# Kernel optimization log

Hardware: AMD Instinct MI355X
Metric: run time of the kernel (lower is better)

The kernel has to match this reference:

```python
import jax, jax.numpy as jnp
import numpy as np

B, TE, TD, H = 8, 512, 256, 256  # batch, enc len, dec len, hidden (He==Hd)

def setup_inputs() -> dict:
    key = jax.random.key(0)
    k1, k2, k3, k4, k5 = jax.random.split(key, 5)
    # Keras 'uniform' initializer: U(-0.05, 0.05)
    u = lambda k, s: jax.random.uniform(k, s, jnp.float32, -0.05, 0.05)
    return {
        "encoder_out_seq": jax.random.normal(k1, (B, TE, H), jnp.float32),
        "decoder_out_seq": jax.random.normal(k2, (B, TD, H), jnp.float32),
        "W_a": u(k3, (H, H)),
        "U_a": u(k4, (H, H)),
        "V_a": u(k5, (H, 1)),
    }

def reference(encoder_out_seq, decoder_out_seq, W_a, U_a, V_a):
    # Bahdanau additive attention, fully batched (same math as the per-step K.rnn loop)
    We = jnp.einsum('bih,hk->bik', encoder_out_seq, W_a)   # [B,Te,H]
    Uh = jnp.einsum('bjh,hk->bjk', decoder_out_seq, U_a)   # [B,Td,H]
    # energies: V_a^T tanh(We_i + Uh_j)  -> [B,Td,Te]
    t = jnp.tanh(We[:, None, :, :] + Uh[:, :, None, :])    # [B,Td,Te,H]
    e = jnp.einsum('bjih,h->bji', t, V_a[:, 0])             # [B,Td,Te]
    e = jax.nn.softmax(e, axis=-1)                          # softmax over encoder positions
    c = jnp.einsum('bji,bih->bjh', e, encoder_out_seq)      # [B,Td,H]
    return (c, e)
```

## Files before the change

### kernel.cpp

```cpp
#include <hip/hip_runtime.h>


#define BB 8
#define TE 512
#define TD 256
#define HH 256

#define EXP2F(x) __builtin_amdgcn_exp2f(x)
#define RCPF(x)  __builtin_amdgcn_rcpf(x)
#define KSCALE   2.8853900817779268f
#define NSC      (-2.8853900817779268f)

__global__ __launch_bounds__(256) void k_pre(
    const float* __restrict__ enc, const float* __restrict__ dec,
    const float* __restrict__ Wa,  const float* __restrict__ Ua,
    float* __restrict__ WeT, float* __restrict__ Uh)
{
    const int tid = threadIdx.x;
    const bool is_enc = blockIdx.x < 256;
    const int bi = is_enc ? blockIdx.x : (blockIdx.x - 256);
    const int m0 = (bi >> 2) * 64;
    const int n0 = (bi & 3) * 64;
    const float* X = is_enc ? enc : dec;
    const float* W = is_enc ? Wa : Ua;

    __shared__ float Xs[32][68];
    __shared__ float Ws[32][68];

    const int kq = tid & 7,  xr = tid >> 3;
    const int wk = tid >> 3, wn = (tid & 7) * 8;
    const int tx = tid & 15, ty = tid >> 4;

    float acc[4][4];
    #pragma unroll
    for (int r = 0; r < 4; r++)
        #pragma unroll
        for (int c = 0; c < 4; c++) acc[r][c] = 0.f;

    for (int kc = 0; kc < HH; kc += 32) {
        float4 xa = *(const float4*)(X + (size_t)(m0 + xr) * HH + kc + kq * 4);
        float4 xb = *(const float4*)(X + (size_t)(m0 + xr + 32) * HH + kc + kq * 4);
        float4 wa = *(const float4*)(W + (size_t)(kc + wk) * HH + n0 + wn);
        float4 wb = *(const float4*)(W + (size_t)(kc + wk) * HH + n0 + wn + 4);
        __syncthreads();
        Xs[kq * 4 + 0][xr] = xa.x; Xs[kq * 4 + 1][xr] = xa.y;
        Xs[kq * 4 + 2][xr] = xa.z; Xs[kq * 4 + 3][xr] = xa.w;
        Xs[kq * 4 + 0][xr + 32] = xb.x; Xs[kq * 4 + 1][xr + 32] = xb.y;
        Xs[kq * 4 + 2][xr + 32] = xb.z; Xs[kq * 4 + 3][xr + 32] = xb.w;
        *(float4*)&Ws[wk][wn]     = wa;
        *(float4*)&Ws[wk][wn + 4] = wb;
        __syncthreads();
        #pragma unroll
        for (int k = 0; k < 32; k++) {
            float4 a = *(const float4*)&Xs[k][ty * 4];
            float4 b = *(const float4*)&Ws[k][tx * 4];
            acc[0][0] = fmaf(a.x, b.x, acc[0][0]); acc[0][1] = fmaf(a.x, b.y, acc[0][1]);
            acc[0][2] = fmaf(a.x, b.z, acc[0][2]); acc[0][3] = fmaf(a.x, b.w, acc[0][3]);
            acc[1][0] = fmaf(a.y, b.x, acc[1][0]); acc[1][1] = fmaf(a.y, b.y, acc[1][1]);
            acc[1][2] = fmaf(a.y, b.z, acc[1][2]); acc[1][3] = fmaf(a.y, b.w, acc[1][3]);
            acc[2][0] = fmaf(a.z, b.x, acc[2][0]); acc[2][1] = fmaf(a.z, b.y, acc[2][1]);
            acc[2][2] = fmaf(a.z, b.z, acc[2][2]); acc[2][3] = fmaf(a.z, b.w, acc[2][3]);
            acc[3][0] = fmaf(a.w, b.x, acc[3][0]); acc[3][1] = fmaf(a.w, b.y, acc[3][1]);
            acc[3][2] = fmaf(a.w, b.z, acc[3][2]); acc[3][3] = fmaf(a.w, b.w, acc[3][3]);
        }
    }

    if (is_enc) {
        const int b  = m0 >> 9;
        const int ib = (m0 & 511) + ty * 4;
        #pragma unroll
        for (int c = 0; c < 4; c++) {
            float4 v;
            v.x = EXP2F(acc[0][c] * KSCALE); v.y = EXP2F(acc[1][c] * KSCALE);
            v.z = EXP2F(acc[2][c] * KSCALE); v.w = EXP2F(acc[3][c] * KSCALE);
            *(float4*)(WeT + ((size_t)b * HH + n0 + tx * 4 + c) * TE + ib) = v;
        }
    } else {
        #pragma unroll
        for (int r = 0; r < 4; r++) {
            float4 v;
            v.x = EXP2F(acc[r][0] * KSCALE); v.y = EXP2F(acc[r][1] * KSCALE);
            v.z = EXP2F(acc[r][2] * KSCALE); v.w = EXP2F(acc[r][3] * KSCALE);
            *(float4*)(Uh + (size_t)(m0 + ty * 4 + r) * HH + n0 + tx * 4) = v;
        }
    }
}

__global__ __launch_bounds__(512) void k_attn(
    const float* __restrict__ enc, const float* __restrict__ WeT,
    const float* __restrict__ Uhe, const float* __restrict__ Va,
    float* __restrict__ out_c, float* __restrict__ out_e)
{
    const int wv = threadIdx.x >> 6, lane = threadIdx.x & 63;
    const int b   = blockIdx.x >> 6;
    const int j0  = (blockIdx.x & 63) * 4;
    const int jj0 = b * TD + j0;

    __shared__ float sP[TE][4];
    __shared__ float sR[8][4][HH];

    const int i = (wv << 6) + lane;
    const float* wt = WeT + (size_t)b * HH * TE + i;
    const float* ut = Uhe + (size_t)jj0 * HH;

    float a0 = 0.f, a1 = 0.f, a2 = 0.f, a3 = 0.f;
    #pragma unroll 4
    for (int h = 0; h < HH; h++) {
        float vah = Va[h];
        float u_0 = ut[h];
        float u_1 = ut[HH + h];
        float u_2 = ut[2 * HH + h];
        float u_3 = ut[3 * HH + h];
        float w = wt[(size_t)h * TE];
        a0 = fmaf(vah, RCPF(fmaf(w, u_0, 1.f)), a0);
        a1 = fmaf(vah, RCPF(fmaf(w, u_1, 1.f)), a1);
        a2 = fmaf(vah, RCPF(fmaf(w, u_2, 1.f)), a2);
        a3 = fmaf(vah, RCPF(fmaf(w, u_3, 1.f)), a3);
    }
    float4 E; E.x = NSC * a0; E.y = NSC * a1; E.z = NSC * a2; E.w = NSC * a3;
    *(float4*)&sP[i][0] = E;
    __syncthreads();

    if (wv < 4) {
        float ev[8];
        float m = -3.0e38f;
        #pragma unroll
        for (int k = 0; k < 8; k++) {
            ev[k] = sP[lane + 64 * k][wv];
            m = fmaxf(m, ev[k]);
        }
        #pragma unroll
        for (int off = 32; off; off >>= 1) m = fmaxf(m, __shfl_xor(m, off, 64));
        float s = 0.f;
        #pragma unroll
        for (int k = 0; k < 8; k++) { ev[k] = EXP2F(ev[k] - m); s += ev[k]; }
        #pragma unroll
        for (int off = 32; off; off >>= 1) s += __shfl_xor(s, off, 64);
        float rs = RCPF(s);
        float* oe = out_e + (size_t)(jj0 + wv) * TE;
        #pragma unroll
        for (int k = 0; k < 8; k++) {
            float p = ev[k] * rs;
            sP[lane + 64 * k][wv] = p;
            oe[lane + 64 * k] = p;
        }
    }
    __syncthreads();

    const float* eb = enc + ((size_t)b * TE + (wv << 6)) * HH + 4 * lane;
    float4 c0 = {0,0,0,0}, c1 = {0,0,0,0}, c2 = {0,0,0,0}, c3 = {0,0,0,0};
    #pragma unroll 2
    for (int k = 0; k < 64; k++) {
        float4 p = *(const float4*)&sP[(wv << 6) + k][0];
        float4 q = *(const float4*)(eb + (size_t)k * HH);
        c0.x = fmaf(p.x, q.x, c0.x); c0.y = fmaf(p.x, q.y, c0.y);
        c0.z = fmaf(p.x, q.z, c0.z); c0.w = fmaf(p.x, q.w, c0.w);
        c1.x = fmaf(p.y, q.x, c1.x); c1.y = fmaf(p.y, q.y, c1.y);
        c1.z = fmaf(p.y, q.z, c1.z); c1.w = fmaf(p.y, q.w, c1.w);
        c2.x = fmaf(p.z, q.x, c2.x); c2.y = fmaf(p.z, q.y, c2.y);
        c2.z = fmaf(p.z, q.z, c2.z); c2.w = fmaf(p.z, q.w, c2.w);
        c3.x = fmaf(p.w, q.x, c3.x); c3.y = fmaf(p.w, q.y, c3.y);
        c3.z = fmaf(p.w, q.z, c3.z); c3.w = fmaf(p.w, q.w, c3.w);
    }
    *(float4*)&sR[wv][0][4 * lane] = c0;
    *(float4*)&sR[wv][1][4 * lane] = c1;
    *(float4*)&sR[wv][2][4 * lane] = c2;
    *(float4*)&sR[wv][3][4 * lane] = c3;
    __syncthreads();

    {
        const int jr = wv & 3;
        const int h2 = (wv >> 2) * 128 + 2 * lane;
        float sx = 0.f, sy = 0.f;
        #pragma unroll
        for (int ww = 0; ww < 8; ww++) {
            float2 t = *(const float2*)&sR[ww][jr][h2];
            sx += t.x; sy += t.y;
        }
        float2 o; o.x = sx; o.y = sy;
        *(float2*)(out_c + (size_t)(jj0 + jr) * HH + h2) = o;
    }
}

extern "C" void kernel_launch(void* const* d_in, const int* in_sizes, int n_in,
                              void* d_out, int out_size, void* d_ws, size_t ws_size,
                              hipStream_t stream) {
    const float* enc = (const float*)d_in[0];
    const float* dec = (const float*)d_in[1];
    const float* Wa  = (const float*)d_in[2];
    const float* Ua  = (const float*)d_in[3];
    const float* Va  = (const float*)d_in[4];

    float* WeT = (float*)d_ws;
    float* Uhe = WeT + (size_t)BB * HH * TE;

    float* out_c = (float*)d_out;
    float* out_e = out_c + (size_t)BB * TD * HH;

    k_pre<<<384, 256, 0, stream>>>(enc, dec, Wa, Ua, WeT, Uhe);
    k_attn<<<BB * TD / 4, 512, 0, stream>>>(enc, WeT, Uhe, Va, out_c, out_e);
}
```

Measured before the change: 126.5 us.

## Interleave WeT in float4 h-groups and split H reduction across doubled waves

```diff
diff --git a/kernel.cpp b/kernel.cpp
--- a/kernel.cpp
+++ b/kernel.cpp
@@ -14,7 +14,7 @@
 __global__ __launch_bounds__(256) void k_pre(
     const float* __restrict__ enc, const float* __restrict__ dec,
     const float* __restrict__ Wa,  const float* __restrict__ Ua,
-    float* __restrict__ WeT, float* __restrict__ Uh)
+    float* __restrict__ W4, float* __restrict__ Uhe)
 {
     const int tid = threadIdx.x;
     const bool is_enc = blockIdx.x < 256;
@@ -68,26 +68,28 @@
     if (is_enc) {
         const int b  = m0 >> 9;
         const int ib = (m0 & 511) + ty * 4;
-        #pragma unroll
-        for (int c = 0; c < 4; c++) {
-            float4 v;
-            v.x = EXP2F(acc[0][c] * KSCALE); v.y = EXP2F(acc[1][c] * KSCALE);
-            v.z = EXP2F(acc[2][c] * KSCALE); v.w = EXP2F(acc[3][c] * KSCALE);
-            *(float4*)(WeT + ((size_t)b * HH + n0 + tx * 4 + c) * TE + ib) = v;
-        }
-    } else {
+        const int hq = (n0 >> 2) + tx;
+        float* dst = W4 + (((size_t)b * 64 + hq) * TE + ib) * 4;
         #pragma unroll
         for (int r = 0; r < 4; r++) {
             float4 v;
             v.x = EXP2F(acc[r][0] * KSCALE); v.y = EXP2F(acc[r][1] * KSCALE);
             v.z = EXP2F(acc[r][2] * KSCALE); v.w = EXP2F(acc[r][3] * KSCALE);
-            *(float4*)(Uh + (size_t)(m0 + ty * 4 + r) * HH + n0 + tx * 4) = v;
+            *(float4*)(dst + (size_t)r * 4) = v;
+        }
+    } else {
+        #pragma unroll
+        for (int r = 0; r < 4; r++) {
+            float4 v;
+            v.x = EXP2F(acc[r][0] * KSCALE); v.y = EXP2F(acc[r][1] * KSCALE);
+            v.z = EXP2F(acc[r][2] * KSCALE); v.w = EXP2F(acc[r][3] * KSCALE);
+            *(float4*)(Uhe + (size_t)(m0 + ty * 4 + r) * HH + n0 + tx * 4) = v;
         }
     }
 }
 
-__global__ __launch_bounds__(512) void k_attn(
-    const float* __restrict__ enc, const float* __restrict__ WeT,
+__global__ __launch_bounds__(1024, 8) void k_attn(
+    const float* __restrict__ enc, const float* __restrict__ W4,
     const float* __restrict__ Uhe, const float* __restrict__ Va,
     float* __restrict__ out_c, float* __restrict__ out_e)
 {
@@ -96,29 +98,45 @@
     const int j0  = (blockIdx.x & 63) * 4;
     const int jj0 = b * TD + j0;
 
-    __shared__ float sP[TE][4];
+    __shared__ float sE[2][TE][4];
     __shared__ float sR[8][4][HH];
 
-    const int i = (wv << 6) + lane;
-    const float* wt = WeT + (size_t)b * HH * TE + i;
-    const float* ut = Uhe + (size_t)jj0 * HH;
+    const int g   = wv >> 3;
+    const int i   = ((wv & 7) << 6) + lane;
+    const int hq0 = g * 32;
+
+    const float* wp = W4 + (((size_t)b * 64 + hq0) * TE + i) * 4;
+    const float* ua = Uhe + (size_t)jj0 * HH + hq0 * 4;
+    const float* va = Va + hq0 * 4;
 
     float a0 = 0.f, a1 = 0.f, a2 = 0.f, a3 = 0.f;
     #pragma unroll 4
-    for (int h = 0; h < HH; h++) {
-        float vah = Va[h];
-        float u_0 = ut[h];
-        float u_1 = ut[HH + h];
-        float u_2 = ut[2 * HH + h];
-        float u_3 = ut[3 * HH + h];
-        float w = wt[(size_t)h * TE];
-        a0 = fmaf(vah, RCPF(fmaf(w, u_0, 1.f)), a0);
-        a1 = fmaf(vah, RCPF(fmaf(w, u_1, 1.f)), a1);
-        a2 = fmaf(vah, RCPF(fmaf(w, u_2, 1.f)), a2);
-        a3 = fmaf(vah, RCPF(fmaf(w, u_3, 1.f)), a3);
+    for (int q = 0; q < 32; q++) {
+        float4 w4 = *(const float4*)(wp + (size_t)q * TE * 4);
+        float4 v4 = *(const float4*)(va + 4 * q);
+        float4 u0 = *(const float4*)(ua + 4 * q);
+        float4 u1 = *(const float4*)(ua + HH + 4 * q);
+        float4 u2 = *(const float4*)(ua + 2 * HH + 4 * q);
+        float4 u3 = *(const float4*)(ua + 3 * HH + 4 * q);
+        a0 = fmaf(v4.x, RCPF(fmaf(w4.x, u0.x, 1.f)), a0);
+        a0 = fmaf(v4.y, RCPF(fmaf(w4.y, u0.y, 1.f)), a0);
+        a0 = fmaf(v4.z, RCPF(fmaf(w4.z, u0.z, 1.f)), a0);
+        a0 = fmaf(v4.w, RCPF(fmaf(w4.w, u0.w, 1.f)), a0);
+        a1 = fmaf(v4.x, RCPF(fmaf(w4.x, u1.x, 1.f)), a1);
+        a1 = fmaf(v4.y, RCPF(fmaf(w4.y, u1.y, 1.f)), a1);
+        a1 = fmaf(v4.z, RCPF(fmaf(w4.z, u1.z, 1.f)), a1);
+        a1 = fmaf(v4.w, RCPF(fmaf(w4.w, u1.w, 1.f)), a1);
+        a2 = fmaf(v4.x, RCPF(fmaf(w4.x, u2.x, 1.f)), a2);
+        a2 = fmaf(v4.y, RCPF(fmaf(w4.y, u2.y, 1.f)), a2);
+        a2 = fmaf(v4.z, RCPF(fmaf(w4.z, u2.z, 1.f)), a2);
+        a2 = fmaf(v4.w, RCPF(fmaf(w4.w, u2.w, 1.f)), a2);
+        a3 = fmaf(v4.x, RCPF(fmaf(w4.x, u3.x, 1.f)), a3);
+        a3 = fmaf(v4.y, RCPF(fmaf(w4.y, u3.y, 1.f)), a3);
+        a3 = fmaf(v4.z, RCPF(fmaf(w4.z, u3.z, 1.f)), a3);
+        a3 = fmaf(v4.w, RCPF(fmaf(w4.w, u3.w, 1.f)), a3);
     }
     float4 E; E.x = NSC * a0; E.y = NSC * a1; E.z = NSC * a2; E.w = NSC * a3;
-    *(float4*)&sP[i][0] = E;
+    *(float4*)&sE[g][i][0] = E;
     __syncthreads();
 
     if (wv < 4) {
@@ -126,7 +144,8 @@
         float m = -3.0e38f;
         #pragma unroll
         for (int k = 0; k < 8; k++) {
-            ev[k] = sP[lane + 64 * k][wv];
+            int ii = lane + 64 * k;
+            ev[k] = sE[0][ii][wv] + sE[1][ii][wv];
             m = fmaxf(m, ev[k]);
         }
         #pragma unroll
@@ -141,17 +160,18 @@
         #pragma unroll
         for (int k = 0; k < 8; k++) {
             float p = ev[k] * rs;
-            sP[lane + 64 * k][wv] = p;
+            sE[0][lane + 64 * k][wv] = p;
             oe[lane + 64 * k] = p;
         }
     }
     __syncthreads();
 
-    const float* eb = enc + ((size_t)b * TE + (wv << 6)) * HH + 4 * lane;
+    const int ib = wv << 5;
+    const float* eb = enc + ((size_t)b * TE + ib) * HH + 4 * lane;
     float4 c0 = {0,0,0,0}, c1 = {0,0,0,0}, c2 = {0,0,0,0}, c3 = {0,0,0,0};
     #pragma unroll 2
-    for (int k = 0; k < 64; k++) {
-        float4 p = *(const float4*)&sP[(wv << 6) + k][0];
+    for (int k = 0; k < 32; k++) {
+        float4 p = *(const float4*)&sE[0][ib + k][0];
         float4 q = *(const float4*)(eb + (size_t)k * HH);
         c0.x = fmaf(p.x, q.x, c0.x); c0.y = fmaf(p.x, q.y, c0.y);
         c0.z = fmaf(p.x, q.z, c0.z); c0.w = fmaf(p.x, q.w, c0.w);
@@ -162,13 +182,31 @@
         c3.x = fmaf(p.w, q.x, c3.x); c3.y = fmaf(p.w, q.y, c3.y);
         c3.z = fmaf(p.w, q.z, c3.z); c3.w = fmaf(p.w, q.w, c3.w);
     }
-    *(float4*)&sR[wv][0][4 * lane] = c0;
-    *(float4*)&sR[wv][1][4 * lane] = c1;
-    *(float4*)&sR[wv][2][4 * lane] = c2;
-    *(float4*)&sR[wv][3][4 * lane] = c3;
-    __syncthreads();
-
-    {
+    if (wv < 8) {
+        *(float4*)&sR[wv][0][4 * lane] = c0;
+        *(float4*)&sR[wv][1][4 * lane] = c1;
+        *(float4*)&sR[wv][2][4 * lane] = c2;
+        *(float4*)&sR[wv][3][4 * lane] = c3;
+    }
+    __syncthreads();
+    if (wv >= 8) {
+        const int w8 = wv - 8;
+        float4 t;
+        t = *(const float4*)&sR[w8][0][4 * lane];
+        t.x += c0.x; t.y += c0.y; t.z += c0.z; t.w += c0.w;
+        *(float4*)&sR[w8][0][4 * lane] = t;
+        t = *(const float4*)&sR[w8][1][4 * lane];
+        t.x += c1.x; t.y += c1.y; t.z += c1.z; t.w += c1.w;
+        *(float4*)&sR[w8][1][4 * lane] = t;
+        t = *(const float4*)&sR[w8][2][4 * lane];
+        t.x += c2.x; t.y += c2.y; t.z += c2.z; t.w += c2.w;
+        *(float4*)&sR[w8][2][4 * lane] = t;
+        t = *(const float4*)&sR[w8][3][4 * lane];
+        t.x += c3.x; t.y += c3.y; t.z += c3.z; t.w += c3.w;
+        *(float4*)&sR[w8][3][4 * lane] = t;
+    }
+    __syncthreads();
+    if (wv < 8) {
         const int jr = wv & 3;
         const int h2 = (wv >> 2) * 128 + 2 * lane;
         float sx = 0.f, sy = 0.f;
@@ -191,12 +229,12 @@
     const float* Ua  = (const float*)d_in[3];
     const float* Va  = (const float*)d_in[4];
 
-    float* WeT = (float*)d_ws;
-    float* Uhe = WeT + (size_t)BB * HH * TE;
+    float* W4  = (float*)d_ws;
+    float* Uhe = W4 + (size_t)BB * HH * TE;
 
     float* out_c = (float*)d_out;
     float* out_e = out_c + (size_t)BB * TD * HH;
 
-    k_pre<<<384, 256, 0, stream>>>(enc, dec, Wa, Ua, WeT, Uhe);
-    k_attn<<<BB * TD / 4, 512, 0, stream>>>(enc, WeT, Uhe, Va, out_c, out_e);
+    k_pre<<<384, 256, 0, stream>>>(enc, dec, Wa, Ua, W4, Uhe);
+    k_attn<<<BB * TD / 4, 1024, 0, stream>>>(enc, W4, Uhe, Va, out_c, out_e);
 }
```

Result: slower. 189.8 us (+50.0%).

## Combine four reciprocal terms per division and use packed float2 FMAs

Applied to the files above, without the earlier changes.

```diff
diff --git a/kernel.cpp b/kernel.cpp
--- a/kernel.cpp
+++ b/kernel.cpp
@@ -11,10 +11,12 @@
 #define KSCALE   2.8853900817779268f
 #define NSC      (-2.8853900817779268f)
 
+typedef float v2f __attribute__((ext_vector_type(2)));
+
 __global__ __launch_bounds__(256) void k_pre(
     const float* __restrict__ enc, const float* __restrict__ dec,
     const float* __restrict__ Wa,  const float* __restrict__ Ua,
-    float* __restrict__ WeT, float* __restrict__ Uh)
+    float* __restrict__ W4, float* __restrict__ Uhe4)
 {
     const int tid = threadIdx.x;
     const bool is_enc = blockIdx.x < 256;
@@ -68,56 +70,83 @@
     if (is_enc) {
         const int b  = m0 >> 9;
         const int ib = (m0 & 511) + ty * 4;
+        const int hq = (n0 >> 2) + tx;
+        float* dst = W4 + (((size_t)b * 64 + hq) * TE + ib) * 4;
+        #pragma unroll
+        for (int r = 0; r < 4; r++) {
+            float4 v;
+            v.x = EXP2F(acc[r][0] * KSCALE); v.y = EXP2F(acc[r][1] * KSCALE);
+            v.z = EXP2F(acc[r][2] * KSCALE); v.w = EXP2F(acc[r][3] * KSCALE);
+            *(float4*)(dst + (size_t)r * 4) = v;
+        }
+    } else {
+        const int qd = (m0 + ty * 4) >> 2;
         #pragma unroll
         for (int c = 0; c < 4; c++) {
             float4 v;
             v.x = EXP2F(acc[0][c] * KSCALE); v.y = EXP2F(acc[1][c] * KSCALE);
             v.z = EXP2F(acc[2][c] * KSCALE); v.w = EXP2F(acc[3][c] * KSCALE);
-            *(float4*)(WeT + ((size_t)b * HH + n0 + tx * 4 + c) * TE + ib) = v;
-        }
-    } else {
-        #pragma unroll
-        for (int r = 0; r < 4; r++) {
-            float4 v;
-            v.x = EXP2F(acc[r][0] * KSCALE); v.y = EXP2F(acc[r][1] * KSCALE);
-            v.z = EXP2F(acc[r][2] * KSCALE); v.w = EXP2F(acc[r][3] * KSCALE);
-            *(float4*)(Uh + (size_t)(m0 + ty * 4 + r) * HH + n0 + tx * 4) = v;
-        }
-    }
+            *(float4*)(Uhe4 + ((size_t)qd * HH + n0 + tx * 4 + c) * 4) = v;
+        }
+    }
+}
+
+__device__ __forceinline__ v2f qstep2(const float4& w4, const float4& v4,
+                                      v2f u0, v2f u1, v2f u2, v2f u3, v2f acc)
+{
+    const v2f one = {1.f, 1.f};
+    v2f A = __builtin_elementwise_fma((v2f)(w4.x), u0, one);
+    v2f B = __builtin_elementwise_fma((v2f)(w4.y), u1, one);
+    v2f C = __builtin_elementwise_fma((v2f)(w4.z), u2, one);
+    v2f D = __builtin_elementwise_fma((v2f)(w4.w), u3, one);
+    v2f dAB = A * B, dCD = C * D;
+    v2f nAB = __builtin_elementwise_fma((v2f)(v4.x), B, (v2f)(v4.y) * A);
+    v2f nCD = __builtin_elementwise_fma((v2f)(v4.z), D, (v2f)(v4.w) * C);
+    v2f num = __builtin_elementwise_fma(nAB, dCD, nCD * dAB);
+    v2f den = dAB * dCD;
+    v2f r; r.x = RCPF(den.x); r.y = RCPF(den.y);
+    return __builtin_elementwise_fma(num, r, acc);
 }
 
 __global__ __launch_bounds__(512) void k_attn(
-    const float* __restrict__ enc, const float* __restrict__ WeT,
-    const float* __restrict__ Uhe, const float* __restrict__ Va,
+    const float* __restrict__ enc, const float* __restrict__ W4,
+    const float* __restrict__ Uhe4, const float* __restrict__ Va,
     float* __restrict__ out_c, float* __restrict__ out_e)
 {
     const int wv = threadIdx.x >> 6, lane = threadIdx.x & 63;
-    const int b   = blockIdx.x >> 6;
-    const int j0  = (blockIdx.x & 63) * 4;
+    const int b   = blockIdx.x & 7;
+    const int j0  = (blockIdx.x >> 3) * 4;
     const int jj0 = b * TD + j0;
 
     __shared__ float sP[TE][4];
     __shared__ float sR[8][4][HH];
 
     const int i = (wv << 6) + lane;
-    const float* wt = WeT + (size_t)b * HH * TE + i;
-    const float* ut = Uhe + (size_t)jj0 * HH;
-
-    float a0 = 0.f, a1 = 0.f, a2 = 0.f, a3 = 0.f;
-    #pragma unroll 4
-    for (int h = 0; h < HH; h++) {
-        float vah = Va[h];
-        float u_0 = ut[h];
-        float u_1 = ut[HH + h];
-        float u_2 = ut[2 * HH + h];
-        float u_3 = ut[3 * HH + h];
-        float w = wt[(size_t)h * TE];
-        a0 = fmaf(vah, RCPF(fmaf(w, u_0, 1.f)), a0);
-        a1 = fmaf(vah, RCPF(fmaf(w, u_1, 1.f)), a1);
-        a2 = fmaf(vah, RCPF(fmaf(w, u_2, 1.f)), a2);
-        a3 = fmaf(vah, RCPF(fmaf(w, u_3, 1.f)), a3);
-    }
-    float4 E; E.x = NSC * a0; E.y = NSC * a1; E.z = NSC * a2; E.w = NSC * a3;
+    const float* wp = W4 + ((size_t)b * 64 * TE + i) * 4;
+    const float4* up = (const float4*)(Uhe4 + (size_t)(jj0 >> 2) * HH * 4);
+    const float4* vp = (const float4*)Va;
+
+    v2f a01 = {0.f, 0.f}, a23 = {0.f, 0.f};
+
+    #pragma unroll 2
+    for (int q = 0; q < 64; q++) {
+        float4 w4 = *(const float4*)(wp + (size_t)q * TE * 4);
+        float4 v4 = vp[q];
+        float4 uh0 = up[4 * q + 0];
+        float4 uh1 = up[4 * q + 1];
+        float4 uh2 = up[4 * q + 2];
+        float4 uh3 = up[4 * q + 3];
+        v2f u0p, u1p, u2p, u3p;
+        u0p.x = uh0.x; u0p.y = uh0.y; u1p.x = uh1.x; u1p.y = uh1.y;
+        u2p.x = uh2.x; u2p.y = uh2.y; u3p.x = uh3.x; u3p.y = uh3.y;
+        a01 = qstep2(w4, v4, u0p, u1p, u2p, u3p, a01);
+        u0p.x = uh0.z; u0p.y = uh0.w; u1p.x = uh1.z; u1p.y = uh1.w;
+        u2p.x = uh2.z; u2p.y = uh2.w; u3p.x = uh3.z; u3p.y = uh3.w;
+        a23 = qstep2(w4, v4, u0p, u1p, u2p, u3p, a23);
+    }
+
+    float4 E;
+    E.x = NSC * a01.x; E.y = NSC * a01.y; E.z = NSC * a23.x; E.w = NSC * a23.y;
     *(float4*)&sP[i][0] = E;
     __syncthreads();
 
@@ -147,25 +176,36 @@
     }
     __syncthreads();
 
-    const float* eb = enc + ((size_t)b * TE + (wv << 6)) * HH + 4 * lane;
-    float4 c0 = {0,0,0,0}, c1 = {0,0,0,0}, c2 = {0,0,0,0}, c3 = {0,0,0,0};
+    const int ib = wv << 6;
+    const float* eb = enc + ((size_t)b * TE + ib) * HH + 4 * lane;
+    v2f cx01 = {0,0}, cy01 = {0,0}, cz01 = {0,0}, cw01 = {0,0};
+    v2f cx23 = {0,0}, cy23 = {0,0}, cz23 = {0,0}, cw23 = {0,0};
     #pragma unroll 2
     for (int k = 0; k < 64; k++) {
-        float4 p = *(const float4*)&sP[(wv << 6) + k][0];
+        float4 p4 = *(const float4*)&sP[ib + k][0];
+        v2f p01; p01.x = p4.x; p01.y = p4.y;
+        v2f p23; p23.x = p4.z; p23.y = p4.w;
         float4 q = *(const float4*)(eb + (size_t)k * HH);
-        c0.x = fmaf(p.x, q.x, c0.x); c0.y = fmaf(p.x, q.y, c0.y);
-        c0.z = fmaf(p.x, q.z, c0.z); c0.w = fmaf(p.x, q.w, c0.w);
-        c1.x = fmaf(p.y, q.x, c1.x); c1.y = fmaf(p.y, q.y, c1.y);
-        c1.z = fmaf(p.y, q.z, c1.z); c1.w = fmaf(p.y, q.w, c1.w);
-        c2.x = fmaf(p.z, q.x, c2.x); c2.y = fmaf(p.z, q.y, c2.y);
-        c2.z = fmaf(p.z, q.z, c2.z); c2.w = fmaf(p.z, q.w, c2.w);
-        c3.x = fmaf(p.w, q.x, c3.x); c3.y = fmaf(p.w, q.y, c3.y);
-        c3.z = fmaf(p.w, q.z, c3.z); c3.w = fmaf(p.w, q.w, c3.w);
-    }
-    *(float4*)&sR[wv][0][4 * lane] = c0;
-    *(float4*)&sR[wv][1][4 * lane] = c1;
-    *(float4*)&sR[wv][2][4 * lane] = c2;
-    *(float4*)&sR[wv][3][4 * lane] = c3;
+        cx01 = __builtin_elementwise_fma(p01, (v2f)(q.x), cx01);
+        cy01 = __builtin_elementwise_fma(p01, (v2f)(q.y), cy01);
+        cz01 = __builtin_elementwise_fma(p01, (v2f)(q.z), cz01);
+        cw01 = __builtin_elementwise_fma(p01, (v2f)(q.w), cw01);
+        cx23 = __builtin_elementwise_fma(p23, (v2f)(q.x), cx23);
+        cy23 = __builtin_elementwise_fma(p23, (v2f)(q.y), cy23);
+        cz23 = __builtin_elementwise_fma(p23, (v2f)(q.z), cz23);
+        cw23 = __builtin_elementwise_fma(p23, (v2f)(q.w), cw23);
+    }
+    {
+        float4 c0, c1, c2, c3;
+        c0.x = cx01.x; c0.y = cy01.x; c0.z = cz01.x; c0.w = cw01.x;
+        c1.x = cx01.y; c1.y = cy01.y; c1.z = cz01.y; c1.w = cw01.y;
+        c2.x = cx23.x; c2.y = cy23.x; c2.z = cz23.x; c2.w = cw23.x;
+        c3.x = cx23.y; c3.y = cy23.y; c3.z = cz23.y; c3.w = cw23.y;
+        *(float4*)&sR[wv][0][4 * lane] = c0;
+        *(float4*)&sR[wv][1][4 * lane] = c1;
+        *(float4*)&sR[wv][2][4 * lane] = c2;
+        *(float4*)&sR[wv][3][4 * lane] = c3;
+    }
     __syncthreads();
 
     {
@@ -191,12 +231,12 @@
     const float* Ua  = (const float*)d_in[3];
     const float* Va  = (const float*)d_in[4];
 
-    float* WeT = (float*)d_ws;
-    float* Uhe = WeT + (size_t)BB * HH * TE;
+    float* W4   = (float*)d_ws;
+    float* Uhe4 = W4 + (size_t)BB * HH * TE;
 
     float* out_c = (float*)d_out;
     float* out_e = out_c + (size_t)BB * TD * HH;
 
-    k_pre<<<384, 256, 0, stream>>>(enc, dec, Wa, Ua, WeT, Uhe);
-    k_attn<<<BB * TD / 4, 512, 0, stream>>>(enc, WeT, Uhe, Va, out_c, out_e);
-}
+    k_pre<<<384, 256, 0, stream>>>(enc, dec, Wa, Ua, W4, Uhe4);
+    k_attn<<<BB * TD / 4, 512, 0, stream>>>(enc, W4, Uhe4, Va, out_c, out_e);
+}
```

Result: faster. 114.9 us (-9.1%).
